# Kernel optimization log

Hardware: AMD Instinct MI355X
Metric: run time of the kernel (lower is better)

Reference implementation:

```python
import jax, jax.numpy as jnp
import numpy as np

B, T, D, F, E, TOP_K = 4, 1024, 1024, 4096, 8, 2


def setup_inputs() -> dict:
    key = jax.random.key(0)
    k0, k1, k2, k3, k4 = jax.random.split(key, 5)
    x = jax.random.normal(k0, (B, T, D), dtype=jnp.float32)
    # xavier-uniform-ish scales
    Wr = jax.random.normal(k1, (D, E), dtype=jnp.float32) * (1.0 / np.sqrt(D))
    W1 = jax.random.normal(k2, (E, D, F), dtype=jnp.float32) * (1.0 / np.sqrt(D))
    W3 = jax.random.normal(k3, (E, D, F), dtype=jnp.float32) * (1.0 / np.sqrt(D))
    W2 = jax.random.normal(k4, (E, F, D), dtype=jnp.float32) * (1.0 / np.sqrt(F))
    return {"x": x, "Wr": Wr, "W1": W1, "W3": W3, "W2": W2}


def reference(x, Wr, W1, W3, W2):
    # Router: logits [B,T,E]
    logits = jnp.einsum('btd,de->bte', x, Wr)
    top_vals, top_idx = jax.lax.top_k(logits, TOP_K)          # [B,T,K]
    weights = jax.nn.softmax(top_vals, axis=-1)               # [B,T,K]
    probs = jax.nn.softmax(logits, axis=-1)                   # [B,T,E]
    usage = probs.mean(axis=(0, 1))                           # [E]
    load_balancing_loss = E * jnp.sum(usage ** 2)

    # SwiGLU experts computed densely per expert: down(silu(gate(x)) * up(x))
    gate = jnp.einsum('btd,edf->ebtf', x, W1)                 # [E,B,T,F]
    up = jnp.einsum('btd,edf->ebtf', x, W3)
    h = jax.nn.silu(gate) * up
    eout = jnp.einsum('ebtf,efd->ebtd', h, W2)                # [E,B,T,D]
    eout = jnp.moveaxis(eout, 0, 2)                           # [B,T,E,D]

    # Gather selected experts and combine with softmax weights
    sel = jnp.take_along_axis(eout, top_idx[..., None], axis=2)  # [B,T,K,D]
    output = jnp.sum(sel * weights[..., None], axis=2)           # [B,T,D]
    return output, load_balancing_loss
```

## Files before the change

### kernel.cpp

```cpp
#include <hip/hip_runtime.h>
#include <hip/hip_bf16.h>
#include <stdint.h>
#include <math.h>

#define NTOK 4096
#define DDIM 1024
#define FDIM 4096
#define NEXP 8
#define NPAIR 8192

#define BM 256
#define BN 64
#define BK 64

#define RT_TPW 8
#define RT_BLOCKS (NTOK / (4 * RT_TPW))

using short8 = __attribute__((ext_vector_type(8))) short;
using f32x4  = __attribute__((ext_vector_type(4))) float;

__device__ __forceinline__ uint16_t f2bf(float f) {
    union { float f; uint32_t u; } v; v.f = f;
    uint32_t r = v.u + 0x7FFFu + ((v.u >> 16) & 1u);
    return (uint16_t)(r >> 16);
}

__device__ __forceinline__ void async16(const void* g, void* l) {
    __builtin_amdgcn_global_load_lds((const __attribute__((address_space(1))) void*)g,
                                     (__attribute__((address_space(3))) void*)l,
                                     16, 0, 0);
}

__global__ void router_kernel(const float* __restrict__ x, const float* __restrict__ Wr,
                              int* __restrict__ cnt_part, float* __restrict__ us_part,
                              int* __restrict__ top_e, float* __restrict__ top_w) {
    __shared__ float us[NEXP];
    __shared__ int cs[NEXP];
    const int tid = threadIdx.x;
    const int wv = tid >> 6;
    const int lane = tid & 63;
    if (tid < NEXP) { us[tid] = 0.f; cs[tid] = 0; }
    __syncthreads();

    for (int i = 0; i < RT_TPW; i++) {
        const int t = blockIdx.x * (4 * RT_TPW) + wv * RT_TPW + i;
        float acc[NEXP];
#pragma unroll
        for (int e = 0; e < NEXP; e++) acc[e] = 0.f;
        const float* xr = x + (size_t)t * DDIM;
        for (int d = lane; d < DDIM; d += 64) {
            float xv = xr[d];
            const float* wr = Wr + (size_t)d * NEXP;
#pragma unroll
            for (int e = 0; e < NEXP; e++) acc[e] += xv * wr[e];
        }
#pragma unroll
        for (int e = 0; e < NEXP; e++) {
#pragma unroll
            for (int off = 32; off > 0; off >>= 1) acc[e] += __shfl_xor(acc[e], off, 64);
        }
        if (lane == 0) {
            int i0 = 0;
#pragma unroll
            for (int e = 1; e < NEXP; e++) if (acc[e] > acc[i0]) i0 = e;
            int i1 = -1;
#pragma unroll
            for (int e = 0; e < NEXP; e++) {
                if (e == i0) continue;
                if (i1 < 0 || acc[e] > acc[i1]) i1 = e;
            }
            float v0 = acc[i0], v1 = acc[i1];
            float e1 = __expf(v1 - v0);
            float inv = 1.f / (1.f + e1);
            top_e[t * 2 + 0] = i0; top_e[t * 2 + 1] = i1;
            top_w[t * 2 + 0] = inv; top_w[t * 2 + 1] = e1 * inv;
            atomicAdd(&cs[i0], 1);
            atomicAdd(&cs[i1], 1);
            float m = acc[0];
#pragma unroll
            for (int e = 1; e < NEXP; e++) m = fmaxf(m, acc[e]);
            float p[NEXP]; float s = 0.f;
#pragma unroll
            for (int e = 0; e < NEXP; e++) { p[e] = __expf(acc[e] - m); s += p[e]; }
            float is = 1.f / s;
#pragma unroll
            for (int e = 0; e < NEXP; e++) atomicAdd(&us[e], p[e] * is);
        }
    }
    __syncthreads();
    if (tid < NEXP) {
        cnt_part[blockIdx.x * NEXP + tid] = cs[tid];
        us_part[blockIdx.x * NEXP + tid] = us[tid];
    }
}

__global__ void finalize_kernel(const int* __restrict__ cnt_part, const float* __restrict__ us_part,
                                int* __restrict__ counts, int* __restrict__ offs,
                                float* __restrict__ out) {
    __shared__ int c[NEXP];
    __shared__ float u[NEXP];
    const int tid = threadIdx.x;
    if (tid < NEXP) {
        int csum = 0; float usum = 0.f;
        for (int b = 0; b < RT_BLOCKS; b++) {
            csum += cnt_part[b * NEXP + tid];
            usum += us_part[b * NEXP + tid];
        }
        counts[tid] = csum; c[tid] = csum; u[tid] = usum;
    }
    __syncthreads();
    if (tid == 0) {
        int s = 0; float l = 0.f;
#pragma unroll
        for (int e = 0; e < NEXP; e++) {
            offs[e] = s; s += c[e];
            float uu = u[e] * (1.f / (float)NTOK);
            l += uu * uu;
        }
        out[(size_t)NTOK * DDIM] = (float)NEXP * l;
    }
}

__global__ void xcast_kernel(const float* __restrict__ x, uint16_t* __restrict__ xb) {
    int i = blockIdx.x * 256 + threadIdx.x;
    float4 v = ((const float4*)x)[i];
    ushort4 o;
    o.x = f2bf(v.x); o.y = f2bf(v.y); o.z = f2bf(v.z); o.w = f2bf(v.w);
    ((ushort4*)xb)[i] = o;
}

__global__ void transpose_cast_kernel(const float* __restrict__ in, uint16_t* __restrict__ outp,
                                      int R, int C, int sel) {
    __shared__ uint16_t tile[64 * 64];
    const int e = blockIdx.z;
    const float* src = in + (size_t)e * R * C;
    const size_t osz = (size_t)R * C * (sel < 0 ? 1 : 2);
    uint16_t* dst = outp + (size_t)e * osz;
    const int r0 = blockIdx.y * 64, c0 = blockIdx.x * 64;
    const int t = threadIdx.x;
    {
        const int rb = t >> 4;
        const int c4 = t & 15;
#pragma unroll
        for (int i = 0; i < 4; i++) {
            const int r = rb + i * 16;
            float4 v = *(const float4*)(src + (size_t)(r0 + r) * C + c0 + c4 * 4);
            const int rc = (r >> 3);
            const int re = (r & 7);
#pragma unroll
            for (int j = 0; j < 4; j++) {
                const int c = c4 * 4 + j;
                float fv = (j == 0) ? v.x : (j == 1) ? v.y : (j == 2) ? v.z : v.w;
                tile[c * 64 + ((rc ^ (c & 7)) << 3) + re] = f2bf(fv);
            }
        }
    }
    __syncthreads();
    {
        const int cr = t >> 3;
        const int ch = t & 7;
#pragma unroll
        for (int i = 0; i < 2; i++) {
            const int c = cr + i * 32;
            uint4 v = *(const uint4*)&tile[c * 64 + ((ch ^ (c & 7)) << 3)];
            const int oc = c0 + c;
            const int orow = (sel < 0) ? oc : (((oc >> 4) << 5) + sel + (oc & 15));
            *(uint4*)(dst + (size_t)orow * R + r0 + ch * 8) = v;
        }
    }
}

__global__ void scatter_kernel(const int* __restrict__ top_e, const float* __restrict__ top_w,
                               const int* __restrict__ offs, int* __restrict__ fill,
                               int* __restrict__ pair_tok, float* __restrict__ pair_w) {
    __shared__ int lcnt[NEXP];
    __shared__ int lbase[NEXP];
    const int tid = threadIdx.x;
    const int t = blockIdx.x * 256 + tid;
    if (tid < NEXP) lcnt[tid] = 0;
    __syncthreads();
    int e0 = top_e[t * 2 + 0], e1 = top_e[t * 2 + 1];
    int r0 = atomicAdd(&lcnt[e0], 1);
    int r1 = atomicAdd(&lcnt[e1], 1);
    __syncthreads();
    if (tid < NEXP) lbase[tid] = atomicAdd(&fill[tid], lcnt[tid]);
    __syncthreads();
    int p0 = offs[e0] + lbase[e0] + r0;
    int p1 = offs[e1] + lbase[e1] + r1;
    pair_tok[p0] = t; pair_w[p0] = top_w[t * 2 + 0];
    pair_tok[p1] = t; pair_w[p1] = top_w[t * 2 + 1];
}

__global__ __launch_bounds__(512, 2)
void expert_up_kernel(const uint16_t* __restrict__ x_bf,
                      const uint16_t* __restrict__ W13t,
                      const int* __restrict__ counts, const int* __restrict__ offs,
                      const int* __restrict__ pair_tok, uint16_t* __restrict__ h) {
    const int e = blockIdx.z;
    const int tile = blockIdx.y;
    const int cntAll = counts[e];
    if (tile * 256 >= cntAll) return;
    const int cnt = min(256, cntAll - tile * 256);
    const int pairBase = offs[e] + tile * 256;
    const int bx = blockIdx.x;

    __shared__ uint16_t smem[4 * 16384];

    const int tid = threadIdx.x;
    const int w = tid >> 6, lane = tid & 63;
    const int wr = w >> 2, wc = w & 3;
    const int lr = lane & 15, q = lane >> 4;
    const int qa = q ^ ((lr >> 1) & 3);
    const int aoff = (wr * 128 + lr) * 32 + qa * 8;
    const int boff = (wc * 64 + lr) * 32 + qa * 8;
    const int q_src = (tid & 3) ^ ((tid >> 3) & 3);
    const int ldst = tid * 8;

    const int tok0 = pair_tok[pairBase + min(tid >> 2, cnt - 1)];
    const int tok1 = pair_tok[pairBase + min(128 + (tid >> 2), cnt - 1)];
    const uint16_t* asrc0 = x_bf + (size_t)tok0 * DDIM + q_src * 8;
    const uint16_t* asrc1 = x_bf + (size_t)tok1 * DDIM + q_src * 8;
    const uint16_t* bsrc = W13t + (size_t)e * 2 * FDIM * DDIM
                         + (size_t)(bx * 256 + (tid >> 2)) * DDIM + q_src * 8;

#define UP_STAGE_A(kt_) do { const int sb = ((kt_) & 3) * 16384; \
    async16(asrc0 + (kt_) * 32, &smem[sb + ldst]); \
    async16(asrc1 + (kt_) * 32, &smem[sb + 4096 + ldst]); } while (0)
#define UP_STAGE_B(kt_) do { const int sb = ((kt_) & 3) * 16384 + 8192; \
    async16(bsrc + (kt_) * 32, &smem[sb + ldst]); \
    async16(bsrc + 131072 + (kt_) * 32, &smem[sb + 4096 + ldst]); } while (0)

    f32x4 acc[8][4];
#pragma unroll
    for (int i = 0; i < 8; i++)
#pragma unroll
        for (int j = 0; j < 4; j++) acc[i][j] = (f32x4){0.f, 0.f, 0.f, 0.f};

    UP_STAGE_A(0); UP_STAGE_B(0);
    UP_STAGE_A(1); UP_STAGE_B(1);
    UP_STAGE_A(2); UP_STAGE_B(2);
    asm volatile("s_waitcnt vmcnt(8)" ::: "memory");
    __builtin_amdgcn_s_barrier();

    for (int kt = 0; kt < 32; ++kt) {
        const uint16_t* A = &smem[(kt & 3) * 16384];
        const uint16_t* B = A + 8192;
        short8 bf[4], af[4];
#pragma unroll
        for (int ni = 0; ni < 4; ni++) bf[ni] = *(const short8*)(B + boff + ni * 512);
#pragma unroll
        for (int mi = 0; mi < 4; mi++) af[mi] = *(const short8*)(A + aoff + mi * 512);
        if (kt < 29) UP_STAGE_A(kt + 3);
        __builtin_amdgcn_s_barrier();
        __builtin_amdgcn_s_setprio(1);
#pragma unroll
        for (int ni = 0; ni < 4; ni++)
#pragma unroll
            for (int mi = 0; mi < 4; mi++)
                acc[mi][ni] = __builtin_amdgcn_mfma_f32_16x16x32_bf16(af[mi], bf[ni], acc[mi][ni], 0, 0, 0);
        __builtin_amdgcn_s_setprio(0);
        __builtin_amdgcn_s_barrier();
#pragma unroll
        for (int mi = 0; mi < 4; mi++) af[mi] = *(const short8*)(A + aoff + (mi + 4) * 512);
        if (kt < 29) UP_STAGE_B(kt + 3);
        __builtin_amdgcn_s_barrier();
        __builtin_amdgcn_s_setprio(1);
#pragma unroll
        for (int ni = 0; ni < 4; ni++)
#pragma unroll
            for (int mi = 0; mi < 4; mi++)
                acc[mi + 4][ni] = __builtin_amdgcn_mfma_f32_16x16x32_bf16(af[mi], bf[ni], acc[mi + 4][ni], 0, 0, 0);
        __builtin_amdgcn_s_setprio(0);
        if (kt < 29)       asm volatile("s_waitcnt vmcnt(8)" ::: "memory");
        else if (kt == 29) asm volatile("s_waitcnt vmcnt(4)" ::: "memory");
        else               asm volatile("s_waitcnt vmcnt(0)" ::: "memory");
        __builtin_amdgcn_s_barrier();
    }
#undef UP_STAGE_A
#undef UP_STAGE_B

#pragma unroll
    for (int mi = 0; mi < 8; mi++) {
#pragma unroll
        for (int r = 0; r < 4; r++) {
            const int rowLocal = wr * 128 + mi * 16 + q * 4 + r;
            if (rowLocal < cnt) {
                uint16_t* dst = h + (size_t)(pairBase + rowLocal) * FDIM + bx * 128 + lr;
#pragma unroll
                for (int j = 0; j < 2; j++) {
                    float g = acc[mi][2 * j][r];
                    float u = acc[mi][2 * j + 1][r];
                    float hv = (g / (1.f + __expf(-g))) * u;
                    dst[(wc * 2 + j) * 16] = f2bf(hv);
                }
            }
        }
    }
}

__global__ __launch_bounds__(256, 3)
void expert_down_kernel(const uint16_t* __restrict__ h, const uint16_t* __restrict__ W2t,
                        const int* __restrict__ counts, const int* __restrict__ offs,
                        const int* __restrict__ pair_tok, const float* __restrict__ pair_w,
                        float* __restrict__ out) {
    const int e = blockIdx.z;
    const int tile = blockIdx.y;
    const int n0 = blockIdx.x * BN;
    const int cntAll = counts[e];
    if (tile * BM >= cntAll) return;
    const int cnt = min(BM, cntAll - tile * BM);
    const int pairBase = offs[e] + tile * BM;

    __shared__ uint16_t As[BM * BK];
    __shared__ uint16_t Bs[BN * BK];

    const int tid = threadIdx.x;
    const int wave = tid >> 6;
    const int lane = tid & 63;
    const int quad = lane >> 4;
    const int lr = lane & 15;
    const int sub = lane >> 3;
    const int swoff = (((lane & 7) ^ sub) << 3);

    int hrow[8];
#pragma unroll
    for (int i = 0; i < 8; i++) {
        int row = wave * 64 + i * 8 + sub;
        hrow[i] = pairBase + min(row, cnt - 1);
    }
    const uint16_t* w2p = W2t + (size_t)e * FDIM * DDIM;

    f32x4 acc[4][4];
#pragma unroll
    for (int i = 0; i < 4; i++)
#pragma unroll
        for (int j = 0; j < 4; j++) acc[i][j] = (f32x4){0.f, 0.f, 0.f, 0.f};

    for (int k0 = 0; k0 < FDIM; k0 += BK) {
        __syncthreads();
#pragma unroll
        for (int i = 0; i < 8; i++)
            async16(h + (size_t)hrow[i] * FDIM + k0 + swoff,
                    &As[(wave * 64 + i * 8) * BK] + lane * 8);
#pragma unroll
        for (int j = 0; j < 2; j++) {
            int n = wave * 16 + j * 8 + sub;
            async16(w2p + (size_t)(n0 + n) * FDIM + k0 + swoff,
                    &Bs[(wave * 16 + j * 8) * BK] + lane * 8);
        }
        __syncthreads();
#pragma unroll
        for (int kk = 0; kk < BK; kk += 32) {
            const int lc = (kk >> 3) + quad;
            short8 af[4];
#pragma unroll
            for (int mi = 0; mi < 4; mi++) {
                int R = wave * 64 + mi * 16 + lr;
                af[mi] = *(const short8*)&As[R * BK + ((lc ^ (lr & 7)) << 3)];
            }
#pragma unroll
            for (int ni = 0; ni < 4; ni++) {
                int n = ni * 16 + lr;
                short8 b = *(const short8*)&Bs[n * BK + ((lc ^ (lr & 7)) << 3)];
#pragma unroll
                for (int mi = 0; mi < 4; mi++)
                    acc[mi][ni] = __builtin_amdgcn_mfma_f32_16x16x32_bf16(af[mi], b, acc[mi][ni], 0, 0, 0);
            }
        }
    }
#pragma unroll
    for (int mi = 0; mi < 4; mi++) {
#pragma unroll
        for (int r = 0; r < 4; r++) {
            int rowLocal = wave * 64 + mi * 16 + quad * 4 + r;
            if (rowLocal < cnt) {
                int pi = pairBase + rowLocal;
                int tok = pair_tok[pi];
                float w = pair_w[pi];
                float* dst = out + (size_t)tok * DDIM + n0 + lr;
#pragma unroll
                for (int ni = 0; ni < 4; ni++)
                    atomicAdd(&dst[ni * 16], acc[mi][ni][r] * w);
            }
        }
    }
}

extern "C" void kernel_launch(void* const* d_in, const int* in_sizes, int n_in,
                              void* d_out, int out_size, void* d_ws, size_t ws_size,
                              hipStream_t stream) {
    (void)in_sizes; (void)n_in; (void)ws_size;
    const float* x  = (const float*)d_in[0];
    const float* Wr = (const float*)d_in[1];
    const float* W1 = (const float*)d_in[2];
    const float* W3 = (const float*)d_in[3];
    const float* W2 = (const float*)d_in[4];
    float* out = (float*)d_out;

    char* ws = (char*)d_ws;
    size_t off = 0;
    int*      counts    = (int*)(ws + off);  off += 64;
    int*      offs      = (int*)(ws + off);  off += 64;
    int*      fill      = (int*)(ws + off);  off += 128;
    int*      top_e     = (int*)(ws + off);  off += 4 * NPAIR;
    float*    top_w     = (float*)(ws + off); off += 4 * NPAIR;
    int*      pair_tok  = (int*)(ws + off);  off += 4 * NPAIR;
    float*    pair_w    = (float*)(ws + off); off += 4 * NPAIR;
    int*      cnt_part  = (int*)(ws + off);  off += 4 * RT_BLOCKS * NEXP;
    float*    us_part   = (float*)(ws + off); off += 4 * RT_BLOCKS * NEXP;
    uint16_t* x_bf      = (uint16_t*)(ws + off); off += (size_t)2 * NTOK * DDIM;
    uint16_t* h         = (uint16_t*)(ws + off); off += (size_t)2 * NPAIR * FDIM;
    const size_t wBytes = (size_t)2 * NEXP * DDIM * FDIM;
    uint16_t* W13t = (uint16_t*)(ws + off);
    uint16_t* W2t  = (uint16_t*)(ws + off + 2 * wBytes);

    hipMemsetAsync(ws, 0, 256, stream);
    hipMemsetAsync(d_out, 0, (size_t)out_size * sizeof(float), stream);

    xcast_kernel<<<NTOK * DDIM / 1024, 256, 0, stream>>>(x, x_bf);
    router_kernel<<<RT_BLOCKS, 256, 0, stream>>>(x, Wr, cnt_part, us_part, top_e, top_w);
    finalize_kernel<<<1, 64, 0, stream>>>(cnt_part, us_part, counts, offs, out);
    scatter_kernel<<<NTOK / 256, 256, 0, stream>>>(top_e, top_w, offs, fill, pair_tok, pair_w);

    transpose_cast_kernel<<<dim3(FDIM / 64, DDIM / 64, NEXP), 256, 0, stream>>>(W1, W13t, DDIM, FDIM, 0);
    transpose_cast_kernel<<<dim3(FDIM / 64, DDIM / 64, NEXP), 256, 0, stream>>>(W3, W13t, DDIM, FDIM, 16);
    transpose_cast_kernel<<<dim3(DDIM / 64, FDIM / 64, NEXP), 256, 0, stream>>>(W2, W2t, FDIM, DDIM, -1);

    dim3 gA(2 * FDIM / 256, NTOK / 256, NEXP);
    expert_up_kernel<<<gA, 512, 0, stream>>>(x_bf, W13t, counts, offs, pair_tok, h);
    dim3 gB(DDIM / BN, NTOK / BM, NEXP);
    expert_down_kernel<<<gB, 256, 0, stream>>>(h, W2t, counts, offs, pair_tok, pair_w, out);
}
```

Before: 825.8 us.

## Retile expert GEMMs with larger M tiles and a triple-buffered async pipeline

The up-projection kernel moves to 512-row by 128-column tiles on a 3-stage LDS ring, one barrier per k-step, with the swizzled LDS layout removed. The down-projection kernel drops its two-syncthreads-per-step loop for a 256x128 tile using the same 3-stage async global-to-LDS pipeline and 8x4 MFMA accumulators per wave. The aim is more reuse of weight tiles per load and overlap of loads with MFMA work. In exchange it raises register and LDS use, lowers occupancy, and the unswizzled LDS reads may cause bank conflicts.

```diff
diff --git a/kernel.cpp b/kernel.cpp
--- a/kernel.cpp
+++ b/kernel.cpp
@@ -8,10 +8,6 @@
 #define FDIM 4096
 #define NEXP 8
 #define NPAIR 8192
-
-#define BM 256
-#define BN 64
-#define BK 64
 
 #define RT_TPW 8
 #define RT_BLOCKS (NTOK / (4 * RT_TPW))
@@ -196,39 +192,38 @@
                       const uint16_t* __restrict__ W13t,
                       const int* __restrict__ counts, const int* __restrict__ offs,
                       const int* __restrict__ pair_tok, uint16_t* __restrict__ h) {
-    const int e = blockIdx.z;
-    const int tile = blockIdx.y;
+    const int e = blockIdx.z, mt = blockIdx.y, bx = blockIdx.x;
     const int cntAll = counts[e];
-    if (tile * 256 >= cntAll) return;
-    const int cnt = min(256, cntAll - tile * 256);
-    const int pairBase = offs[e] + tile * 256;
-    const int bx = blockIdx.x;
-
-    __shared__ uint16_t smem[4 * 16384];
+    if (mt * 512 >= cntAll) return;
+    const int cnt = min(512, cntAll - mt * 512);
+    const int pairBase = offs[e] + mt * 512;
+
+    __shared__ uint16_t smem[3 * 20480];
 
     const int tid = threadIdx.x;
     const int w = tid >> 6, lane = tid & 63;
-    const int wr = w >> 2, wc = w & 3;
+    const int wr = w >> 1, wc = w & 1;
     const int lr = lane & 15, q = lane >> 4;
-    const int qa = q ^ ((lr >> 1) & 3);
-    const int aoff = (wr * 128 + lr) * 32 + qa * 8;
-    const int boff = (wc * 64 + lr) * 32 + qa * 8;
-    const int q_src = (tid & 3) ^ ((tid >> 3) & 3);
+    const int aoff = (wr * 128 + lr) * 32 + q * 8;
+    const int boff = 16384 + (wc * 64 + lr) * 32 + q * 8;
     const int ldst = tid * 8;
-
-    const int tok0 = pair_tok[pairBase + min(tid >> 2, cnt - 1)];
-    const int tok1 = pair_tok[pairBase + min(128 + (tid >> 2), cnt - 1)];
-    const uint16_t* asrc0 = x_bf + (size_t)tok0 * DDIM + q_src * 8;
-    const uint16_t* asrc1 = x_bf + (size_t)tok1 * DDIM + q_src * 8;
+    const int rowid = tid >> 2, chunk = tid & 3;
+
+    const uint16_t* asrc[4];
+#pragma unroll
+    for (int i = 0; i < 4; i++) {
+        int tok = pair_tok[pairBase + min(i * 128 + rowid, cnt - 1)];
+        asrc[i] = x_bf + (size_t)tok * DDIM + chunk * 8;
+    }
     const uint16_t* bsrc = W13t + (size_t)e * 2 * FDIM * DDIM
-                         + (size_t)(bx * 256 + (tid >> 2)) * DDIM + q_src * 8;
-
-#define UP_STAGE_A(kt_) do { const int sb = ((kt_) & 3) * 16384; \
-    async16(asrc0 + (kt_) * 32, &smem[sb + ldst]); \
-    async16(asrc1 + (kt_) * 32, &smem[sb + 4096 + ldst]); } while (0)
-#define UP_STAGE_B(kt_) do { const int sb = ((kt_) & 3) * 16384 + 8192; \
-    async16(bsrc + (kt_) * 32, &smem[sb + ldst]); \
-    async16(bsrc + 131072 + (kt_) * 32, &smem[sb + 4096 + ldst]); } while (0)
+                         + (size_t)(bx * 128 + rowid) * DDIM + chunk * 8;
+
+#define UST(kt_, sb_) do { \
+    async16(asrc[0] + (kt_) * 32, &smem[(sb_) + ldst]); \
+    async16(asrc[1] + (kt_) * 32, &smem[(sb_) + 4096 + ldst]); \
+    async16(asrc[2] + (kt_) * 32, &smem[(sb_) + 8192 + ldst]); \
+    async16(asrc[3] + (kt_) * 32, &smem[(sb_) + 12288 + ldst]); \
+    async16(bsrc + (kt_) * 32, &smem[(sb_) + 16384 + ldst]); } while (0)
 
     f32x4 acc[8][4];
 #pragma unroll
@@ -236,21 +231,22 @@
 #pragma unroll
         for (int j = 0; j < 4; j++) acc[i][j] = (f32x4){0.f, 0.f, 0.f, 0.f};
 
-    UP_STAGE_A(0); UP_STAGE_B(0);
-    UP_STAGE_A(1); UP_STAGE_B(1);
-    UP_STAGE_A(2); UP_STAGE_B(2);
-    asm volatile("s_waitcnt vmcnt(8)" ::: "memory");
+    UST(0, 0); UST(1, 20480);
+    asm volatile("s_waitcnt vmcnt(5)" ::: "memory");
     __builtin_amdgcn_s_barrier();
 
+    int cur = 0;
     for (int kt = 0; kt < 32; ++kt) {
-        const uint16_t* A = &smem[(kt & 3) * 16384];
-        const uint16_t* B = A + 8192;
+        const uint16_t* A = &smem[cur];
         short8 bf[4], af[4];
 #pragma unroll
-        for (int ni = 0; ni < 4; ni++) bf[ni] = *(const short8*)(B + boff + ni * 512);
+        for (int ni = 0; ni < 4; ni++) bf[ni] = *(const short8*)(A + boff + ni * 512);
 #pragma unroll
         for (int mi = 0; mi < 4; mi++) af[mi] = *(const short8*)(A + aoff + mi * 512);
-        if (kt < 29) UP_STAGE_A(kt + 3);
+        if (kt + 2 < 32) {
+            int stg = cur + 2 * 20480; if (stg >= 3 * 20480) stg -= 3 * 20480;
+            UST(kt + 2, stg);
+        }
         __builtin_amdgcn_s_barrier();
         __builtin_amdgcn_s_setprio(1);
 #pragma unroll
@@ -259,11 +255,8 @@
             for (int mi = 0; mi < 4; mi++)
                 acc[mi][ni] = __builtin_amdgcn_mfma_f32_16x16x32_bf16(af[mi], bf[ni], acc[mi][ni], 0, 0, 0);
         __builtin_amdgcn_s_setprio(0);
-        __builtin_amdgcn_s_barrier();
 #pragma unroll
         for (int mi = 0; mi < 4; mi++) af[mi] = *(const short8*)(A + aoff + (mi + 4) * 512);
-        if (kt < 29) UP_STAGE_B(kt + 3);
-        __builtin_amdgcn_s_barrier();
         __builtin_amdgcn_s_setprio(1);
 #pragma unroll
         for (int ni = 0; ni < 4; ni++)
@@ -271,13 +264,12 @@
             for (int mi = 0; mi < 4; mi++)
                 acc[mi + 4][ni] = __builtin_amdgcn_mfma_f32_16x16x32_bf16(af[mi], bf[ni], acc[mi + 4][ni], 0, 0, 0);
         __builtin_amdgcn_s_setprio(0);
-        if (kt < 29)       asm volatile("s_waitcnt vmcnt(8)" ::: "memory");
-        else if (kt == 29) asm volatile("s_waitcnt vmcnt(4)" ::: "memory");
-        else               asm volatile("s_waitcnt vmcnt(0)" ::: "memory");
+        if (kt + 2 < 32)      asm volatile("s_waitcnt vmcnt(5)" ::: "memory");
+        else if (kt + 1 < 32) asm volatile("s_waitcnt vmcnt(0)" ::: "memory");
         __builtin_amdgcn_s_barrier();
-    }
-#undef UP_STAGE_A
-#undef UP_STAGE_B
+        cur += 20480; if (cur == 3 * 20480) cur = 0;
+    }
+#undef UST
 
 #pragma unroll
     for (int mi = 0; mi < 8; mi++) {
@@ -285,7 +277,7 @@
         for (int r = 0; r < 4; r++) {
             const int rowLocal = wr * 128 + mi * 16 + q * 4 + r;
             if (rowLocal < cnt) {
-                uint16_t* dst = h + (size_t)(pairBase + rowLocal) * FDIM + bx * 128 + lr;
+                uint16_t* dst = h + (size_t)(pairBase + rowLocal) * FDIM + bx * 64 + lr;
 #pragma unroll
                 for (int j = 0; j < 2; j++) {
                     float g = acc[mi][2 * j][r];
@@ -298,89 +290,106 @@
     }
 }
 
-__global__ __launch_bounds__(256, 3)
+__global__ __launch_bounds__(256, 2)
 void expert_down_kernel(const uint16_t* __restrict__ h, const uint16_t* __restrict__ W2t,
                         const int* __restrict__ counts, const int* __restrict__ offs,
                         const int* __restrict__ pair_tok, const float* __restrict__ pair_w,
                         float* __restrict__ out) {
-    const int e = blockIdx.z;
-    const int tile = blockIdx.y;
-    const int n0 = blockIdx.x * BN;
+    const int e = blockIdx.z, mt = blockIdx.y;
+    const int n0 = blockIdx.x * 128;
     const int cntAll = counts[e];
-    if (tile * BM >= cntAll) return;
-    const int cnt = min(BM, cntAll - tile * BM);
-    const int pairBase = offs[e] + tile * BM;
-
-    __shared__ uint16_t As[BM * BK];
-    __shared__ uint16_t Bs[BN * BK];
+    if (mt * 256 >= cntAll) return;
+    const int cnt = min(256, cntAll - mt * 256);
+    const int pairBase = offs[e] + mt * 256;
+
+    __shared__ uint16_t smem[3 * 12288];
 
     const int tid = threadIdx.x;
-    const int wave = tid >> 6;
-    const int lane = tid & 63;
-    const int quad = lane >> 4;
-    const int lr = lane & 15;
-    const int sub = lane >> 3;
-    const int swoff = (((lane & 7) ^ sub) << 3);
-
-    int hrow[8];
-#pragma unroll
-    for (int i = 0; i < 8; i++) {
-        int row = wave * 64 + i * 8 + sub;
-        hrow[i] = pairBase + min(row, cnt - 1);
+    const int w = tid >> 6, lane = tid & 63;
+    const int wr = w >> 1, wc = w & 1;
+    const int lr = lane & 15, q = lane >> 4;
+    const int aoff = (wr * 128 + lr) * 32 + q * 8;
+    const int boff = 8192 + (wc * 64 + lr) * 32 + q * 8;
+    const int ldst = tid * 8;
+    const int rowid = tid >> 2, chunk = tid & 3;
+
+    const uint16_t* asrc[4];
+#pragma unroll
+    for (int i = 0; i < 4; i++) {
+        int pr = pairBase + min(i * 64 + rowid, cnt - 1);
+        asrc[i] = h + (size_t)pr * FDIM + chunk * 8;
     }
     const uint16_t* w2p = W2t + (size_t)e * FDIM * DDIM;
-
-    f32x4 acc[4][4];
-#pragma unroll
-    for (int i = 0; i < 4; i++)
+    const uint16_t* bsrc0 = w2p + (size_t)(n0 + rowid) * FDIM + chunk * 8;
+    const uint16_t* bsrc1 = w2p + (size_t)(n0 + 64 + rowid) * FDIM + chunk * 8;
+
+#define DST_(kt_, sb_) do { \
+    async16(asrc[0] + (kt_) * 32, &smem[(sb_) + ldst]); \
+    async16(asrc[1] + (kt_) * 32, &smem[(sb_) + 2048 + ldst]); \
+    async16(asrc[2] + (kt_) * 32, &smem[(sb_) + 4096 + ldst]); \
+    async16(asrc[3] + (kt_) * 32, &smem[(sb_) + 6144 + ldst]); \
+    async16(bsrc0 + (kt_) * 32, &smem[(sb_) + 8192 + ldst]); \
+    async16(bsrc1 + (kt_) * 32, &smem[(sb_) + 10240 + ldst]); } while (0)
+
+    f32x4 acc[8][4];
+#pragma unroll
+    for (int i = 0; i < 8; i++)
 #pragma unroll
         for (int j = 0; j < 4; j++) acc[i][j] = (f32x4){0.f, 0.f, 0.f, 0.f};
 
-    for (int k0 = 0; k0 < FDIM; k0 += BK) {
-        __syncthreads();
-#pragma unroll
-        for (int i = 0; i < 8; i++)
-            async16(h + (size_t)hrow[i] * FDIM + k0 + swoff,
-                    &As[(wave * 64 + i * 8) * BK] + lane * 8);
-#pragma unroll
-        for (int j = 0; j < 2; j++) {
-            int n = wave * 16 + j * 8 + sub;
-            async16(w2p + (size_t)(n0 + n) * FDIM + k0 + swoff,
-                    &Bs[(wave * 16 + j * 8) * BK] + lane * 8);
-        }
-        __syncthreads();
-#pragma unroll
-        for (int kk = 0; kk < BK; kk += 32) {
-            const int lc = (kk >> 3) + quad;
-            short8 af[4];
-#pragma unroll
-            for (int mi = 0; mi < 4; mi++) {
-                int R = wave * 64 + mi * 16 + lr;
-                af[mi] = *(const short8*)&As[R * BK + ((lc ^ (lr & 7)) << 3)];
-            }
-#pragma unroll
-            for (int ni = 0; ni < 4; ni++) {
-                int n = ni * 16 + lr;
-                short8 b = *(const short8*)&Bs[n * BK + ((lc ^ (lr & 7)) << 3)];
-#pragma unroll
-                for (int mi = 0; mi < 4; mi++)
-                    acc[mi][ni] = __builtin_amdgcn_mfma_f32_16x16x32_bf16(af[mi], b, acc[mi][ni], 0, 0, 0);
-            }
-        }
-    }
-#pragma unroll
-    for (int mi = 0; mi < 4; mi++) {
+    DST_(0, 0); DST_(1, 12288);
+    asm volatile("s_waitcnt vmcnt(6)" ::: "memory");
+    __builtin_amdgcn_s_barrier();
+
+    int cur = 0;
+    for (int kt = 0; kt < 128; ++kt) {
+        const uint16_t* A = &smem[cur];
+        short8 bf[4], af[4];
+#pragma unroll
+        for (int ni = 0; ni < 4; ni++) bf[ni] = *(const short8*)(A + boff + ni * 512);
+#pragma unroll
+        for (int mi = 0; mi < 4; mi++) af[mi] = *(const short8*)(A + aoff + mi * 512);
+        if (kt + 2 < 128) {
+            int stg = cur + 2 * 12288; if (stg >= 3 * 12288) stg -= 3 * 12288;
+            DST_(kt + 2, stg);
+        }
+        __builtin_amdgcn_s_barrier();
+        __builtin_amdgcn_s_setprio(1);
+#pragma unroll
+        for (int ni = 0; ni < 4; ni++)
+#pragma unroll
+            for (int mi = 0; mi < 4; mi++)
+                acc[mi][ni] = __builtin_amdgcn_mfma_f32_16x16x32_bf16(af[mi], bf[ni], acc[mi][ni], 0, 0, 0);
+        __builtin_amdgcn_s_setprio(0);
+#pragma unroll
+        for (int mi = 0; mi < 4; mi++) af[mi] = *(const short8*)(A + aoff + (mi + 4) * 512);
+        __builtin_amdgcn_s_setprio(1);
+#pragma unroll
+        for (int ni = 0; ni < 4; ni++)
+#pragma unroll
+            for (int mi = 0; mi < 4; mi++)
+                acc[mi + 4][ni] = __builtin_amdgcn_mfma_f32_16x16x32_bf16(af[mi], bf[ni], acc[mi + 4][ni], 0, 0, 0);
+        __builtin_amdgcn_s_setprio(0);
+        if (kt + 2 < 128)      asm volatile("s_waitcnt vmcnt(6)" ::: "memory");
+        else if (kt + 1 < 128) asm volatile("s_waitcnt vmcnt(0)" ::: "memory");
+        __builtin_amdgcn_s_barrier();
+        cur += 12288; if (cur == 3 * 12288) cur = 0;
+    }
+#undef DST_
+
+#pragma unroll
+    for (int mi = 0; mi < 8; mi++) {
 #pragma unroll
         for (int r = 0; r < 4; r++) {
-            int rowLocal = wave * 64 + mi * 16 + quad * 4 + r;
+            const int rowLocal = wr * 128 + mi * 16 + q * 4 + r;
             if (rowLocal < cnt) {
                 int pi = pairBase + rowLocal;
                 int tok = pair_tok[pi];
-                float w = pair_w[pi];
-                float* dst = out + (size_t)tok * DDIM + n0 + lr;
+                float wgt = pair_w[pi];
+                float* dst = out + (size_t)tok * DDIM + n0 + wc * 64 + lr;
 #pragma unroll
                 for (int ni = 0; ni < 4; ni++)
-                    atomicAdd(&dst[ni * 16], acc[mi][ni][r] * w);
+                    atomicAdd(&dst[ni * 16], acc[mi][ni][r] * wgt);
             }
         }
     }
@@ -426,8 +435,8 @@
     transpose_cast_kernel<<<dim3(FDIM / 64, DDIM / 64, NEXP), 256, 0, stream>>>(W3, W13t, DDIM, FDIM, 16);
     transpose_cast_kernel<<<dim3(DDIM / 64, FDIM / 64, NEXP), 256, 0, stream>>>(W2, W2t, FDIM, DDIM, -1);
 
-    dim3 gA(2 * FDIM / 256, NTOK / 256, NEXP);
+    dim3 gA(2 * FDIM / 128, NTOK / 512, NEXP);
     expert_up_kernel<<<gA, 512, 0, stream>>>(x_bf, W13t, counts, offs, pair_tok, h);
-    dim3 gB(DDIM / BN, NTOK / BM, NEXP);
+    dim3 gB(DDIM / 128, NTOK / 256, NEXP);
     expert_down_kernel<<<gB, 256, 0, stream>>>(h, W2t, counts, offs, pair_tok, pair_w, out);
 }
```

Result: slower. 842.6 us (+2.0%).
